# Performance work log

Measured on AMD Instinct MI355X. Metric: run time of the kernel, lower is better.

Reference implementation:

```python
import jax, jax.numpy as jnp
import numpy as np


def _dct2(x):
    """DCT-II over last dim, scipy norm=None scaling (matches the torch rfft trick:
    X_k = 2 * sum_n x_n cos(pi*k*(2n+1)/(2N))). Expressed as one batched matmul."""
    N = x.shape[-1]
    n = jnp.arange(N, dtype=x.dtype)
    k = jnp.arange(N, dtype=x.dtype)
    # D[k, n] = 2*cos(pi*k*(2n+1)/(2N))
    D = 2.0 * jnp.cos((np.pi / (2.0 * N)) * k[:, None] * (2.0 * n[None, :] + 1.0))
    return jnp.einsum('kn,bcn->bck', D, x)


def setup_inputs() -> dict:
    key = jax.random.key(0)
    k0, k1, k2 = jax.random.split(key, 3)
    b, c, l = 32, 512, 1024
    x = jax.random.normal(k0, (b, c, l), dtype=jnp.float32)
    # 1x1 Conv1d weights (kernel_size=1, bias=False) stored as [out, in]
    w1 = jax.random.normal(k1, (2 * c, c), dtype=jnp.float32) / np.float32(np.sqrt(c))
    w2 = jax.random.normal(k2, (c, 2 * c), dtype=jnp.float32) / np.float32(np.sqrt(2 * c))
    ln_w = jnp.ones((l,), dtype=jnp.float32)
    ln_b = jnp.zeros((l,), dtype=jnp.float32)
    return {"x": x, "w1": w1, "w2": w2, "ln_w": ln_w, "ln_b": ln_b}


def reference(x, w1, w2, ln_w, ln_b):
    eps = 1e-6
    freq = _dct2(x)                                   # [b, c, l]
    mu = jnp.mean(freq, axis=-1, keepdims=True)
    var = jnp.var(freq, axis=-1, keepdims=True)       # biased, like nn.LayerNorm
    h = (freq - mu) * jax.lax.rsqrt(var + eps) * ln_w + ln_b
    # fc: Conv1d(c->2c, k=1) -> Dropout(eval: identity) -> ReLU -> Conv1d(2c->c) -> Sigmoid
    h = jax.nn.relu(jnp.einsum('oi,bil->bol', w1, h))  # [b, 2c, l]
    gate = jax.nn.sigmoid(jnp.einsum('oi,bil->bol', w2, h))  # [b, c, l]
    return x * gate
```

## Files before the change

### kernel.cpp

```cpp
#include <hip/hip_runtime.h>
#include <hip/hip_bf16.h>
#include <math.h>

typedef short short8 __attribute__((ext_vector_type(8)));
typedef short short4v __attribute__((ext_vector_type(4)));
typedef float f32x4 __attribute__((ext_vector_type(4)));

__device__ __forceinline__ short f2bf(float f) {
  union { float f; unsigned u; } v; v.f = f;
  unsigned r = v.u + 0x7FFFu + ((v.u >> 16) & 1u);
  return (short)(r >> 16);
}
__device__ __forceinline__ float bf2f(short s) {
  union { unsigned u; float f; } v; v.u = ((unsigned)(unsigned short)s) << 16;
  return v.f;
}

__global__ __launch_bounds__(256) void cast_w(const float* __restrict__ w1,
                                              const float* __restrict__ w2,
                                              short* __restrict__ w1_bf,
                                              short* __restrict__ w2_bf) {
  int i = blockIdx.x * blockDim.x + threadIdx.x;
  const float* src = (i < 131072) ? w1 : w2;
  short* dst = (i < 131072) ? w1_bf : w2_bf;
  int j = (i < 131072) ? i : i - 131072;
  float4 v = ((const float4*)src)[j];
  short4v o;
  o.x = f2bf(v.x); o.y = f2bf(v.y); o.z = f2bf(v.z); o.w = f2bf(v.w);
  ((short4v*)dst)[j] = o;
}

__global__ __launch_bounds__(256) void prep_eo(const float* __restrict__ x,
                                               short* __restrict__ eo) {
  int t = blockIdx.x * 256 + threadIdx.x;
  int bc = t >> 7, n0 = (t & 127) * 4;
  const float* xr = x + (size_t)bc * 1024;
  float4 f = *(const float4*)(xr + n0);
  float4 r = *(const float4*)(xr + 1020 - n0);
  short4v ef, of;
  ef.x = f2bf(f.x + r.w); ef.y = f2bf(f.y + r.z); ef.z = f2bf(f.z + r.y); ef.w = f2bf(f.w + r.x);
  of.x = f2bf(f.x - r.w); of.y = f2bf(f.y - r.z); of.z = f2bf(f.z - r.y); of.w = f2bf(f.w - r.x);
  *(short4v*)&eo[(size_t)bc * 512 + n0] = ef;
  *(short4v*)&eo[8388608 + (size_t)bc * 512 + n0] = of;
}

__global__ __launch_bounds__(256) void build_Deo(short* __restrict__ D) {
  int t = blockIdx.x * 256 + threadIdx.x;
  int parity = t >> 18, rem = t & 262143;
  int k2 = rem >> 9, n = rem & 511;
  const float s = 1.5339807878856412e-03f;
  float arg = (s * (float)(2 * k2 + parity)) * (float)(2 * n + 1);
  D[t] = f2bf(2.0f * cosf(arg));
}

__global__ __launch_bounds__(256) void ln_stats(const float2* __restrict__ partial,
                                                float2* __restrict__ musd) {
  int n = blockIdx.x * 256 + threadIdx.x;
  float S = 0.f, Q = 0.f;
#pragma unroll
  for (int r = 0; r < 4; ++r) {
    float2 p = partial[(size_t)r * 16384 + n];
    S += p.x; Q += p.y;
  }
  float mu  = S * (1.f / 1024.f);
  float var = Q * (1.f / 1024.f) - mu * mu;
  float2 o; o.x = mu; o.y = rsqrtf(var + 1e-6f);
  musd[n] = o;
}

__global__ __launch_bounds__(256) void ln_apply(short* __restrict__ freqT,
                                                const float2* __restrict__ musd,
                                                const float* __restrict__ lnw,
                                                const float* __restrict__ lnb) {
  int t = blockIdx.x * 256 + threadIdx.x;
  int c8 = t & 63;
  int k  = (t >> 6) & 1023;
  int b  = t >> 16;
  size_t idx = ((size_t)b << 19) + (size_t)k * 512 + (size_t)c8 * 8;
  short8 v = *(const short8*)&freqT[idx];
  float w  = lnw[k];
  float bb = lnb[k];
  const float2* ms = &musd[b * 512 + c8 * 8];
  short8 o;
#pragma unroll
  for (int j = 0; j < 8; ++j) {
    float f = bf2f(v[j]);
    float2 m = ms[j];
    o[j] = f2bf((f - m.x) * m.y * w + bb);
  }
  *(short8*)&freqT[idx] = o;
}

template<int EPI>
__global__ __launch_bounds__(256, 2) void gemmF(
    const short* __restrict__ A, const short* __restrict__ B,
    void* __restrict__ Cout, const float* __restrict__ X,
    float2* __restrict__ P, int K, int NT, long strideA, long strideB)
{
  __shared__ short As[2][8192];
  __shared__ short Bs[2][4096];
  const int tid = threadIdx.x;
  const int l   = tid & 63;
  const int w   = tid >> 6;
  const int wm  = w >> 1;
  const int wc  = w & 1;
  const int lr  = l & 15;
  const int lhi = l >> 4;

  const int nwg = gridDim.x, q = nwg >> 3, orig = blockIdx.x;
  const int wgid = (orig & 7) * q + (orig >> 3);
  int bx, by, bz;
  bx = wgid & 1; bz = (wgid >> 1) & 1; by = wgid >> 2;

  const long row0 = (long)bx * 256, col0 = (long)by * 128;
  const short* Ab = A + (size_t)bz * strideA + (size_t)row0 * K;
  const short* Bb = B + (size_t)bz * strideB + (size_t)col0 * K;

  const int sx    = (lhi ^ ((lr >> 1) & 3)) * 8;
  const int abase = (wm * 128 + lr) * 32;
  const int bbase = (wc * 64  + lr) * 32;

  f32x4 acc[8][4];
#pragma unroll
  for (int i = 0; i < 8; ++i)
#pragma unroll
    for (int j = 0; j < 4; ++j) acc[i][j] = (f32x4){0.f, 0.f, 0.f, 0.f};

#define GLL(SRC, DST) __builtin_amdgcn_global_load_lds(                      \
      (const __attribute__((address_space(1))) void*)(SRC),                  \
      (__attribute__((address_space(3))) void*)(DST), 16, 0, 0)

#define STAGE(KT, D) do {                                                    \
    const size_t kb_ = (size_t)(KT) * 32;                                    \
    _Pragma("unroll")                                                        \
    for (int r_ = 0; r_ < 4; ++r_) {                                         \
      int c_ = r_ * 256 + tid; int row_ = c_ >> 2; int sl_ = c_ & 3;         \
      int sc_ = (sl_ ^ ((row_ >> 1) & 3)) * 8;                               \
      GLL(Ab + (size_t)row_ * K + kb_ + sc_, &As[D][row_ * 32 + sl_ * 8]);   \
    }                                                                        \
    _Pragma("unroll")                                                        \
    for (int r_ = 0; r_ < 2; ++r_) {                                         \
      int c_ = r_ * 256 + tid; int row_ = c_ >> 2; int sl_ = c_ & 3;         \
      int sc_ = (sl_ ^ ((row_ >> 1) & 3)) * 8;                               \
      GLL(Bb + (size_t)row_ * K + kb_ + sc_, &Bs[D][row_ * 32 + sl_ * 8]);   \
    }                                                                        \
  } while (0)

#define LD8(PTR, OFF) (*(const short8*)&(PTR)[OFF])
#define MFMA(AV, BV, C) __builtin_amdgcn_mfma_f32_16x16x32_bf16(AV, BV, C, 0, 0, 0)
#define SBAR __builtin_amdgcn_s_barrier()
#define SCHB __builtin_amdgcn_sched_barrier(0)

#define MROW(MI, AV)                                                         \
    acc[MI][0] = MFMA(AV, b0, acc[MI][0]);                                   \
    acc[MI][1] = MFMA(AV, b1, acc[MI][1]);                                   \
    acc[MI][2] = MFMA(AV, b2, acc[MI][2]);                                   \
    acc[MI][3] = MFMA(AV, b3, acc[MI][3]);

  STAGE(0, 0);
  STAGE(1, 1);

  int cur = 0;
  for (int kt = 0; kt < NT; ++kt) {
    if (kt + 1 < NT) { asm volatile("s_waitcnt vmcnt(6)" ::: "memory"); }
    else             { asm volatile("s_waitcnt vmcnt(0)" ::: "memory"); }
    SCHB; SBAR;
    const short* Ad = As[cur];
    const short* Bd = Bs[cur];
    short8 a0, a1, a2, a3, a4, a5, a6, a7, b0, b1, b2, b3;
    a0 = LD8(Ad, abase + 0 * 512 + sx);
    a1 = LD8(Ad, abase + 1 * 512 + sx);
    b0 = LD8(Bd, bbase + 0 * 512 + sx);
    b1 = LD8(Bd, bbase + 1 * 512 + sx);
    b2 = LD8(Bd, bbase + 2 * 512 + sx);
    b3 = LD8(Bd, bbase + 3 * 512 + sx);
    a2 = LD8(Ad, abase + 2 * 512 + sx);
    a3 = LD8(Ad, abase + 3 * 512 + sx);
    a4 = LD8(Ad, abase + 4 * 512 + sx);
    a5 = LD8(Ad, abase + 5 * 512 + sx);
    a6 = LD8(Ad, abase + 6 * 512 + sx);
    a7 = LD8(Ad, abase + 7 * 512 + sx);
    SCHB;
    asm volatile("s_waitcnt lgkmcnt(6)" ::: "memory");
    SCHB;
    __builtin_amdgcn_s_setprio(1);
    MROW(0, a0) MROW(1, a1)
    __builtin_amdgcn_s_setprio(0);
    SCHB;
    asm volatile("s_waitcnt lgkmcnt(0)" ::: "memory");
    SCHB; SBAR;
    if (kt + 2 < NT) STAGE(kt + 2, cur);
    SCHB;
    __builtin_amdgcn_s_setprio(1);
    MROW(2, a2) MROW(3, a3) MROW(4, a4) MROW(5, a5) MROW(6, a6) MROW(7, a7)
    __builtin_amdgcn_s_setprio(0);
    SCHB;
    cur ^= 1;
  }

  float sv[4], qv[4];
#pragma unroll
  for (int ni = 0; ni < 4; ++ni) { sv[ni] = 0.f; qv[ni] = 0.f; }

#pragma unroll
  for (int mi = 0; mi < 8; ++mi) {
#pragma unroll
    for (int ni = 0; ni < 4; ++ni) {
#pragma unroll
      for (int j = 0; j < 4; ++j) {
        int r  = (int)row0 + wm * 128 + mi * 16 + lhi * 4 + j;
        int cc = (int)col0 + wc * 64 + ni * 16 + lr;
        float v = acc[mi][ni][j];
        sv[ni] += v; qv[ni] += v * v;
        int rr = r * 2 + bz;
        ((short*)Cout)[((size_t)(cc >> 9) << 19) + (size_t)rr * 512 + (cc & 511)] = f2bf(v);
      }
    }
  }

  {
    __syncthreads();
    float* redS = (float*)&As[0][0];
    float* redQ = redS + 1024;
    const int contrib = wm * 4 + lhi;
#pragma unroll
    for (int ni = 0; ni < 4; ++ni) {
      int ccl = wc * 64 + ni * 16 + lr;
      redS[ccl * 8 + contrib] = sv[ni];
      redQ[ccl * 8 + contrib] = qv[ni];
    }
    __syncthreads();
    if (tid < 128) {
      float S = 0.f, Q = 0.f;
#pragma unroll
      for (int i = 0; i < 8; ++i) { S += redS[tid * 8 + i]; Q += redQ[tid * 8 + i]; }
      float2 o; o.x = S; o.y = Q;
      P[(size_t)(bz * 2 + bx) * 16384 + col0 + tid] = o;
    }
  }
#undef MROW
#undef MFMA
#undef LD8
#undef STAGE
#undef GLL
#undef SBAR
#undef SCHB
}

template<int EPI>
__global__ __launch_bounds__(256, 2) void gemm128(
    const short* __restrict__ A, const short* __restrict__ B,
    void* __restrict__ Cout, const float* __restrict__ X,
    int K, int NT, long strideA, long strideB)
{
  __shared__ short As[2][8192];
  __shared__ short Bs[2][8192];
  const int tid = threadIdx.x;
  const int l   = tid & 63;
  const int w   = tid >> 6;
  const int wm  = w >> 1;
  const int wc  = w & 1;
  const int l7  = l & 7;
  const int lr  = l & 15;
  const int lhi = l >> 4;

  const int nwg = gridDim.x, q = nwg >> 3, orig = blockIdx.x;
  const int wgid = (orig & 7) * q + (orig >> 3);
  int bx, by, bz;
  if (EPI == 1) { by = wgid & 7; bx = (wgid >> 3) & 7; bz = wgid >> 6; }
  else          { bx = wgid & 3; by = (wgid >> 2) & 7; bz = wgid >> 5; }

  const long row0 = (long)bx * 128, col0 = (long)by * 128;
  const short* Ab = A + (size_t)bz * strideA + (size_t)row0 * K;
  const short* Bb = B + (size_t)bz * strideB + (size_t)col0 * K;

  const int rowb  = tid >> 3;
  const int colel = ((tid & 7) ^ ((tid >> 3) & 7)) * 8;
  const int abase = (wm * 64 + lr) * 64;
  const int bbase = (wc * 64 + lr) * 64;
  const int s0 = ((lhi    ) ^ l7) * 8;
  const int s1 = ((lhi + 4) ^ l7) * 8;

  f32x4 acc[4][4];
#pragma unroll
  for (int i = 0; i < 4; ++i)
#pragma unroll
    for (int j = 0; j < 4; ++j) acc[i][j] = (f32x4){0.f, 0.f, 0.f, 0.f};

#define GLL(SRC, DST) __builtin_amdgcn_global_load_lds(                      \
      (const __attribute__((address_space(1))) void*)(SRC),                  \
      (__attribute__((address_space(3))) void*)(DST), 16, 0, 0)

#define STAGE(KT, D) do {                                                    \
    const size_t ko_ = (size_t)(KT) * 64 + colel;                            \
    _Pragma("unroll")                                                        \
    for (int r_ = 0; r_ < 4; ++r_)                                           \
      GLL(Ab + (size_t)(r_ * 32 + rowb) * K + ko_,                           \
          &As[D][(r_ * 32 + rowb) * 64 + (tid & 7) * 8]);                    \
    _Pragma("unroll")                                                        \
    for (int r_ = 0; r_ < 4; ++r_)                                           \
      GLL(Bb + (size_t)(r_ * 32 + rowb) * K + ko_,                           \
          &Bs[D][(r_ * 32 + rowb) * 64 + (tid & 7) * 8]);                    \
  } while (0)

#define LD8(PTR, OFF) (*(const short8*)&(PTR)[OFF])
#define MFMA(AV, BV, C) __builtin_amdgcn_mfma_f32_16x16x32_bf16(AV, BV, C, 0, 0, 0)
#define SBAR __builtin_amdgcn_s_barrier()
#define SCHB __builtin_amdgcn_sched_barrier(0)

#define MFMA16(A0, A1, A2, A3, B0, B1, B2, B3)                               \
    __builtin_amdgcn_s_setprio(1);                                           \
    acc[0][0]=MFMA(A0,B0,acc[0][0]); acc[0][1]=MFMA(A0,B1,acc[0][1]);        \
    acc[0][2]=MFMA(A0,B2,acc[0][2]); acc[0][3]=MFMA(A0,B3,acc[0][3]);        \
    acc[1][0]=MFMA(A1,B0,acc[1][0]); acc[1][1]=MFMA(A1,B1,acc[1][1]);        \
    acc[1][2]=MFMA(A1,B2,acc[1][2]); acc[1][3]=MFMA(A1,B3,acc[1][3]);        \
    acc[2][0]=MFMA(A2,B0,acc[2][0]); acc[2][1]=MFMA(A2,B1,acc[2][1]);        \
    acc[2][2]=MFMA(A2,B2,acc[2][2]); acc[2][3]=MFMA(A2,B3,acc[2][3]);        \
    acc[3][0]=MFMA(A3,B0,acc[3][0]); acc[3][1]=MFMA(A3,B1,acc[3][1]);        \
    acc[3][2]=MFMA(A3,B2,acc[3][2]); acc[3][3]=MFMA(A3,B3,acc[3][3]);        \
    __builtin_amdgcn_s_setprio(0);

  STAGE(0, 0);
  STAGE(1, 1);

  int cur = 0;
  for (int kt = 0; kt < NT; ++kt) {
    if (kt + 1 < NT) { asm volatile("s_waitcnt vmcnt(8)" ::: "memory"); }
    else             { asm volatile("s_waitcnt vmcnt(0)" ::: "memory"); }
    SCHB; SBAR;
    const short* Ad = As[cur];
    const short* Bd = Bs[cur];
    short8 a00, a01, a02, a03, b00, b01, b02, b03;
    short8 a10, a11, a12, a13, b10, b11, b12, b13;
    a00 = LD8(Ad, abase + 0 * 1024 + s0);
    a01 = LD8(Ad, abase + 1 * 1024 + s0);
    a02 = LD8(Ad, abase + 2 * 1024 + s0);
    a03 = LD8(Ad, abase + 3 * 1024 + s0);
    b00 = LD8(Bd, bbase + 0 * 1024 + s0);
    b01 = LD8(Bd, bbase + 1 * 1024 + s0);
    b02 = LD8(Bd, bbase + 2 * 1024 + s0);
    b03 = LD8(Bd, bbase + 3 * 1024 + s0);
    a10 = LD8(Ad, abase + 0 * 1024 + s1);
    a11 = LD8(Ad, abase + 1 * 1024 + s1);
    a12 = LD8(Ad, abase + 2 * 1024 + s1);
    a13 = LD8(Ad, abase + 3 * 1024 + s1);
    b10 = LD8(Bd, bbase + 0 * 1024 + s1);
    b11 = LD8(Bd, bbase + 1 * 1024 + s1);
    b12 = LD8(Bd, bbase + 2 * 1024 + s1);
    b13 = LD8(Bd, bbase + 3 * 1024 + s1);
    SCHB;
    asm volatile("s_waitcnt lgkmcnt(8)" ::: "memory");
    SCHB;
    MFMA16(a00, a01, a02, a03, b00, b01, b02, b03)
    SCHB;
    asm volatile("s_waitcnt lgkmcnt(0)" ::: "memory");
    SCHB; SBAR;
    if (kt + 2 < NT) STAGE(kt + 2, cur);
    SCHB;
    MFMA16(a10, a11, a12, a13, b10, b11, b12, b13)
    SCHB;
    cur ^= 1;
  }

#pragma unroll
  for (int mi = 0; mi < 4; ++mi) {
#pragma unroll
    for (int ni = 0; ni < 4; ++ni) {
#pragma unroll
      for (int j = 0; j < 4; ++j) {
        int r  = (int)row0 + wm * 64 + mi * 16 + lhi * 4 + j;
        int cc = (int)col0 + wc * 64 + ni * 16 + lr;
        float v = acc[mi][ni][j];
        if (EPI == 1) {
          ((short*)Cout)[(size_t)bz * 1048576 + (size_t)r * 1024 + cc] = f2bf(v > 0.f ? v : 0.f);
        } else {
          size_t idx = (size_t)bz * 524288 + (size_t)r * 1024 + cc;
          float g = 1.f / (1.f + __expf(-v));
          ((float*)Cout)[idx] = X[idx] * g;
        }
      }
    }
  }
#undef MFMA16
#undef MFMA
#undef LD8
#undef STAGE
#undef GLL
#undef SBAR
#undef SCHB
}

extern "C" void kernel_launch(void* const* d_in, const int* in_sizes, int n_in,
                              void* d_out, int out_size, void* d_ws, size_t ws_size,
                              hipStream_t stream) {
  const float* x    = (const float*)d_in[0];
  const float* w1   = (const float*)d_in[1];
  const float* w2   = (const float*)d_in[2];
  const float* ln_w = (const float*)d_in[3];
  const float* ln_b = (const float*)d_in[4];
  float* out = (float*)d_out;

  char* ws = (char*)d_ws;
  short* Deo    = (short*)(ws);
  short* w1_bf  = (short*)(ws + 1048576);
  short* w2_bf  = (short*)(ws + 2097152);
  short* freqT  = (short*)(ws + 3145728);
  short* z1t    = (short*)(ws + 36700160);
  short* eo     = z1t;
  float2* part  = (float2*)(ws + 103809024);
  float2* musd  = (float2*)(ws + 104857600);

  prep_eo<<<dim3(8192), dim3(256), 0, stream>>>(x, eo);
  cast_w<<<dim3(1024), dim3(256), 0, stream>>>(w1, w2, w1_bf, w2_bf);
  build_Deo<<<dim3(2048), dim3(256), 0, stream>>>(Deo);

  gemmF<0><<<dim3(512), dim3(256), 0, stream>>>(
      Deo, eo, (void*)freqT, nullptr, part, 512, 16, 262144, 8388608);

  ln_stats<<<dim3(64), dim3(256), 0, stream>>>(part, musd);

  ln_apply<<<dim3(8192), dim3(256), 0, stream>>>(freqT, musd, ln_w, ln_b);

  gemm128<1><<<dim3(2048), dim3(256), 0, stream>>>(
      freqT, w1_bf, (void*)z1t, nullptr, 512, 8, 524288, 0);

  gemm128<2><<<dim3(1024), dim3(256), 0, stream>>>(
      w2_bf, z1t, (void*)out, x, 1024, 16, 0, 1048576);
}
```

Before: 159.8 us.

## Replace first FC GEMM with 256x256-tile, 8-wave kernel using split-phase pipelined staging

The first 1x1-conv GEMM (LN output times w1, ReLU, bf16 store) moves from a 128x128 tile with 4 waves to a 256x256 tile with 8 waves (512 threads) and double-buffered 64KB LDS. Global-to-LDS loads are split into half-tiles interleaved across four MFMA quarter-phases with explicit vmcnt waits. The larger tile raises arithmetic intensity and cuts redundant operand reads, and the template GEMMs are split into specialised kernels. The cost is more barriers per k-step and 64KB LDS per block, which limits residency, plus a fragile hand-written schedule.

Result: no change. 158.2 us (median of 2 runs) (-1.0%).

```diff
diff --git a/kernel.cpp b/kernel.cpp
--- a/kernel.cpp
+++ b/kernel.cpp
@@ -91,11 +91,10 @@
   *(short8*)&freqT[idx] = o;
 }
 
-template<int EPI>
-__global__ __launch_bounds__(256, 2) void gemmF(
+__global__ __launch_bounds__(256, 2) void gemm1F(
     const short* __restrict__ A, const short* __restrict__ B,
-    void* __restrict__ Cout, const float* __restrict__ X,
-    float2* __restrict__ P, int K, int NT, long strideA, long strideB)
+    void* __restrict__ Cout, float2* __restrict__ P,
+    int K, int NT, long strideA, long strideB)
 {
   __shared__ short As[2][8192];
   __shared__ short Bs[2][4096];
@@ -109,8 +108,7 @@
 
   const int nwg = gridDim.x, q = nwg >> 3, orig = blockIdx.x;
   const int wgid = (orig & 7) * q + (orig >> 3);
-  int bx, by, bz;
-  bx = wgid & 1; bz = (wgid >> 1) & 1; by = wgid >> 2;
+  int bx = wgid & 1, bz = (wgid >> 1) & 1, by = wgid >> 2;
 
   const long row0 = (long)bx * 256, col0 = (long)by * 128;
   const short* Ab = A + (size_t)bz * strideA + (size_t)row0 * K;
@@ -239,19 +237,154 @@
     }
   }
 #undef MROW
-#undef MFMA
-#undef LD8
 #undef STAGE
-#undef GLL
-#undef SBAR
-#undef SCHB
-}
-
-template<int EPI>
-__global__ __launch_bounds__(256, 2) void gemm128(
+}
+
+__global__ __launch_bounds__(512, 2) void gemm2p8(
     const short* __restrict__ A, const short* __restrict__ B,
-    void* __restrict__ Cout, const float* __restrict__ X,
-    int K, int NT, long strideA, long strideB)
+    short* __restrict__ Cout, int K, int NT, long strideA)
+{
+  __shared__ short As[2][16384];
+  __shared__ short Bs[2][16384];
+  const int tid = threadIdx.x;
+  const int l   = tid & 63;
+  const int w   = tid >> 6;
+  const int wm  = w >> 2;
+  const int wn  = w & 3;
+  const int l7  = l & 7;
+  const int lr  = l & 15;
+  const int lhi = l >> 4;
+
+  const int nwg = gridDim.x, q = nwg >> 3, orig = blockIdx.x;
+  const int wgid = (orig & 7) * q + (orig >> 3);
+  const int bx = wgid & 3, by = (wgid >> 2) & 3, bz = wgid >> 4;
+
+  const long row0 = (long)bx * 256, col0 = (long)by * 256;
+  const short* Ab = A + (size_t)bz * strideA + (size_t)row0 * K;
+  const short* Bb = B + (size_t)col0 * K;
+
+  const int rowb  = w * 8 + (l >> 3);
+  const int colel = (l7 ^ (l >> 3)) * 8;
+  const int abase = (wm * 16 + lr) * 64;
+  const int bbase = (wn * 16 + lr) * 64;
+  const int s0 = ((lhi    ) ^ l7) * 8;
+  const int s1 = ((lhi + 4) ^ l7) * 8;
+
+  f32x4 acc[8][4];
+#pragma unroll
+  for (int i = 0; i < 8; ++i)
+#pragma unroll
+    for (int j = 0; j < 4; ++j) acc[i][j] = (f32x4){0.f, 0.f, 0.f, 0.f};
+
+#define ST_HALF(OPb, OPlds, T, H) do {                                       \
+    const size_t ko_ = (size_t)(T) * 64 + colel;                             \
+    const short* sb_ = (OPb) + (size_t)((H) * 128 + rowb) * K + ko_;         \
+    short* db_ = &OPlds[(T) & 1][(H) * 8192 + w * 512 + l * 8];              \
+    GLL(sb_, db_);                                                           \
+    GLL(sb_ + (size_t)64 * K, db_ + 4096);                                   \
+  } while (0)
+
+#define QUAD16(MIH, A0, A1, A2, A3, B0, B1, B2, B3)                          \
+    __builtin_amdgcn_s_setprio(1);                                           \
+    acc[MIH+0][0]=MFMA(A0,B0,acc[MIH+0][0]); acc[MIH+0][1]=MFMA(A0,B1,acc[MIH+0][1]); \
+    acc[MIH+0][2]=MFMA(A0,B2,acc[MIH+0][2]); acc[MIH+0][3]=MFMA(A0,B3,acc[MIH+0][3]); \
+    acc[MIH+1][0]=MFMA(A1,B0,acc[MIH+1][0]); acc[MIH+1][1]=MFMA(A1,B1,acc[MIH+1][1]); \
+    acc[MIH+1][2]=MFMA(A1,B2,acc[MIH+1][2]); acc[MIH+1][3]=MFMA(A1,B3,acc[MIH+1][3]); \
+    acc[MIH+2][0]=MFMA(A2,B0,acc[MIH+2][0]); acc[MIH+2][1]=MFMA(A2,B1,acc[MIH+2][1]); \
+    acc[MIH+2][2]=MFMA(A2,B2,acc[MIH+2][2]); acc[MIH+2][3]=MFMA(A2,B3,acc[MIH+2][3]); \
+    acc[MIH+3][0]=MFMA(A3,B0,acc[MIH+3][0]); acc[MIH+3][1]=MFMA(A3,B1,acc[MIH+3][1]); \
+    acc[MIH+3][2]=MFMA(A3,B2,acc[MIH+3][2]); acc[MIH+3][3]=MFMA(A3,B3,acc[MIH+3][3]); \
+    __builtin_amdgcn_s_setprio(0);
+
+#define LGKM0 asm volatile("s_waitcnt lgkmcnt(0)" ::: "memory")
+
+  ST_HALF(Bb, Bs, 0, 0); ST_HALF(Bb, Bs, 0, 1);
+  ST_HALF(Ab, As, 0, 0); ST_HALF(Ab, As, 0, 1);
+  ST_HALF(Bb, Bs, 1, 0); ST_HALF(Bb, Bs, 1, 1);
+  ST_HALF(Ab, As, 1, 0);
+  asm volatile("s_waitcnt vmcnt(6)" ::: "memory");
+  SBAR;
+
+  short8 b00, b01, b10, b11, b20, b21, b30, b31;
+  short8 a0, a1, a2, a3;
+  int cur = 0;
+  for (int kt = 0; kt < NT; ++kt) {
+    const short* Ad = As[cur];
+    const short* Bd = Bs[cur];
+
+    a0 = LD8(Ad, 0 * 2048 + abase + s0);
+    a1 = LD8(Ad, 1 * 2048 + abase + s0);
+    a2 = LD8(Ad, 2 * 2048 + abase + s0);
+    a3 = LD8(Ad, 3 * 2048 + abase + s0);
+    b00 = LD8(Bd, bbase + s0);          b01 = LD8(Bd, bbase + s1);
+    b10 = LD8(Bd, 4096 + bbase + s0);   b11 = LD8(Bd, 4096 + bbase + s1);
+    b20 = LD8(Bd, 8192 + bbase + s0);
+    b30 = LD8(Bd, 12288 + bbase + s0);
+    if (kt + 1 < NT) ST_HALF(Ab, As, kt + 1, 1);
+    SCHB; SBAR;
+    LGKM0; SCHB;
+    QUAD16(0, a0, a1, a2, a3, b00, b10, b20, b30)
+    SCHB; SBAR;
+
+    a0 = LD8(Ad, 8192 + 0 * 2048 + abase + s0);
+    a1 = LD8(Ad, 8192 + 1 * 2048 + abase + s0);
+    a2 = LD8(Ad, 8192 + 2 * 2048 + abase + s0);
+    a3 = LD8(Ad, 8192 + 3 * 2048 + abase + s0);
+    b21 = LD8(Bd, 8192 + bbase + s1);
+    b31 = LD8(Bd, 12288 + bbase + s1);
+    if (kt + 2 < NT) ST_HALF(Bb, Bs, kt + 2, 0);
+    SCHB; SBAR;
+    LGKM0; SCHB;
+    QUAD16(4, a0, a1, a2, a3, b00, b10, b20, b30)
+    SCHB; SBAR;
+
+    a0 = LD8(Ad, 0 * 2048 + abase + s1);
+    a1 = LD8(Ad, 1 * 2048 + abase + s1);
+    a2 = LD8(Ad, 2 * 2048 + abase + s1);
+    a3 = LD8(Ad, 3 * 2048 + abase + s1);
+    if (kt + 2 < NT) ST_HALF(Bb, Bs, kt + 2, 1);
+    SCHB; SBAR;
+    LGKM0; SCHB;
+    QUAD16(0, a0, a1, a2, a3, b01, b11, b21, b31)
+    SCHB; SBAR;
+
+    a0 = LD8(Ad, 8192 + 0 * 2048 + abase + s1);
+    a1 = LD8(Ad, 8192 + 1 * 2048 + abase + s1);
+    a2 = LD8(Ad, 8192 + 2 * 2048 + abase + s1);
+    a3 = LD8(Ad, 8192 + 3 * 2048 + abase + s1);
+    if (kt + 2 < NT) ST_HALF(Ab, As, kt + 2, 0);
+    if (kt + 2 < NT)      { asm volatile("s_waitcnt vmcnt(6)" ::: "memory"); }
+    else if (kt + 1 < NT) { asm volatile("s_waitcnt vmcnt(0)" ::: "memory"); }
+    SCHB; SBAR;
+    LGKM0; SCHB;
+    QUAD16(4, a0, a1, a2, a3, b01, b11, b21, b31)
+    SCHB; SBAR;
+
+    cur ^= 1;
+  }
+
+#pragma unroll
+  for (int mi = 0; mi < 8; ++mi) {
+#pragma unroll
+    for (int ni = 0; ni < 4; ++ni) {
+#pragma unroll
+      for (int j = 0; j < 4; ++j) {
+        int r  = (int)row0 + (mi >> 2) * 128 + (mi & 3) * 32 + wm * 16 + lhi * 4 + j;
+        int cc = (int)col0 + (ni >> 1) * 128 + (ni & 1) * 64 + wn * 16 + lr;
+        float v = acc[mi][ni][j];
+        Cout[(size_t)bz * 1048576 + (size_t)r * 1024 + cc] = f2bf(v > 0.f ? v : 0.f);
+      }
+    }
+  }
+#undef QUAD16
+#undef ST_HALF
+#undef LGKM0
+}
+
+__global__ __launch_bounds__(256, 2) void gemm3k(
+    const short* __restrict__ A, const short* __restrict__ B,
+    float* __restrict__ Cout, const float* __restrict__ X,
+    int K, int NT, long strideB)
 {
   __shared__ short As[2][8192];
   __shared__ short Bs[2][8192];
@@ -266,12 +399,10 @@
 
   const int nwg = gridDim.x, q = nwg >> 3, orig = blockIdx.x;
   const int wgid = (orig & 7) * q + (orig >> 3);
-  int bx, by, bz;
-  if (EPI == 1) { by = wgid & 7; bx = (wgid >> 3) & 7; bz = wgid >> 6; }
-  else          { bx = wgid & 3; by = (wgid >> 2) & 7; bz = wgid >> 5; }
+  int bx = wgid & 3, by = (wgid >> 2) & 7, bz = wgid >> 5;
 
   const long row0 = (long)bx * 128, col0 = (long)by * 128;
-  const short* Ab = A + (size_t)bz * strideA + (size_t)row0 * K;
+  const short* Ab = A + (size_t)row0 * K;
   const short* Bb = B + (size_t)bz * strideB + (size_t)col0 * K;
 
   const int rowb  = tid >> 3;
@@ -286,10 +417,6 @@
   for (int i = 0; i < 4; ++i)
 #pragma unroll
     for (int j = 0; j < 4; ++j) acc[i][j] = (f32x4){0.f, 0.f, 0.f, 0.f};
-
-#define GLL(SRC, DST) __builtin_amdgcn_global_load_lds(                      \
-      (const __attribute__((address_space(1))) void*)(SRC),                  \
-      (__attribute__((address_space(3))) void*)(DST), 16, 0, 0)
 
 #define STAGE(KT, D) do {                                                    \
     const size_t ko_ = (size_t)(KT) * 64 + colel;                            \
@@ -302,11 +429,6 @@
       GLL(Bb + (size_t)(r_ * 32 + rowb) * K + ko_,                           \
           &Bs[D][(r_ * 32 + rowb) * 64 + (tid & 7) * 8]);                    \
   } while (0)
-
-#define LD8(PTR, OFF) (*(const short8*)&(PTR)[OFF])
-#define MFMA(AV, BV, C) __builtin_amdgcn_mfma_f32_16x16x32_bf16(AV, BV, C, 0, 0, 0)
-#define SBAR __builtin_amdgcn_s_barrier()
-#define SCHB __builtin_amdgcn_sched_barrier(0)
 
 #define MFMA16(A0, A1, A2, A3, B0, B1, B2, B3)                               \
     __builtin_amdgcn_s_setprio(1);                                           \
@@ -371,21 +493,17 @@
         int r  = (int)row0 + wm * 64 + mi * 16 + lhi * 4 + j;
         int cc = (int)col0 + wc * 64 + ni * 16 + lr;
         float v = acc[mi][ni][j];
-        if (EPI == 1) {
-          ((short*)Cout)[(size_t)bz * 1048576 + (size_t)r * 1024 + cc] = f2bf(v > 0.f ? v : 0.f);
-        } else {
-          size_t idx = (size_t)bz * 524288 + (size_t)r * 1024 + cc;
-          float g = 1.f / (1.f + __expf(-v));
-          ((float*)Cout)[idx] = X[idx] * g;
-        }
+        size_t idx = (size_t)bz * 524288 + (size_t)r * 1024 + cc;
+        float g = 1.f / (1.f + __expf(-v));
+        Cout[idx] = X[idx] * g;
       }
     }
   }
 #undef MFMA16
-#undef MFMA
-#undef LD8
 #undef STAGE
 #undef GLL
+#undef LD8
+#undef MFMA
 #undef SBAR
 #undef SCHB
 }
@@ -414,16 +532,16 @@
   cast_w<<<dim3(1024), dim3(256), 0, stream>>>(w1, w2, w1_bf, w2_bf);
   build_Deo<<<dim3(2048), dim3(256), 0, stream>>>(Deo);
 
-  gemmF<0><<<dim3(512), dim3(256), 0, stream>>>(
-      Deo, eo, (void*)freqT, nullptr, part, 512, 16, 262144, 8388608);
+  gemm1F<<<dim3(512), dim3(256), 0, stream>>>(
+      Deo, eo, (void*)freqT, part, 512, 16, 262144, 8388608);
 
   ln_stats<<<dim3(64), dim3(256), 0, stream>>>(part, musd);
 
   ln_apply<<<dim3(8192), dim3(256), 0, stream>>>(freqT, musd, ln_w, ln_b);
 
-  gemm128<1><<<dim3(2048), dim3(256), 0, stream>>>(
-      freqT, w1_bf, (void*)z1t, nullptr, 512, 8, 524288, 0);
-
-  gemm128<2><<<dim3(1024), dim3(256), 0, stream>>>(
-      w2_bf, z1t, (void*)out, x, 1024, 16, 0, 1048576);
-}
+  gemm2p8<<<dim3(512), dim3(512), 0, stream>>>(
+      freqT, w1_bf, z1t, 512, 8, 524288);
+
+  gemm3k<<<dim3(1024), dim3(256), 0, stream>>>(
+      w2_bf, z1t, out, x, 1024, 16, 1048576);
+}
```
